# Kernel tuning notes

Hardware: AMD Instinct MI355X
Metric: run time of the kernel (lower is better)

The kernel has to match this reference:

```python
import jax, jax.numpy as jnp
import numpy as np

ALPHA = 0.2  # LeakyReLU negative slope
MASK_VAL = -9e15


def setup_inputs() -> dict:
    key = jax.random.key(0)
    k1, k2, k3, k4 = jax.random.split(key, 4)
    N, F_in, F_out = 8192, 512, 128
    h = jax.random.normal(k1, (N, F_in), dtype=jnp.float32)
    adj = jax.random.randint(k2, (N, N), 0, 2, dtype=jnp.int32)
    w = jax.random.normal(k3, (F_in, F_out), dtype=jnp.float32) * 0.05
    a = jax.random.normal(k4, (2 * F_out, 1), dtype=jnp.float32) * 0.05
    return {"h": h, "adj": adj, "w": w, "a": a}


def reference(h, adj, w, a):
    F_out = w.shape[1]
    Wh = h @ w                                  # [N, F_out]
    Wh1 = Wh @ a[:F_out, :]                     # [N, 1]
    Wh2 = Wh @ a[F_out:, :]                     # [N, 1]
    e = Wh1 + Wh2.T                             # [N, N] broadcast additive score
    e = jnp.where(e > 0, e, ALPHA * e)          # LeakyReLU
    att = jnp.where(adj > 0, e, MASK_VAL)       # mask non-edges
    att = jax.nn.softmax(att, axis=1)           # row softmax
    # dropout is identity in eval mode
    h_prime = att @ Wh                          # [N, F_out]
    return jax.nn.elu(h_prime)                  # concat=True -> ELU
```

## Files before the change

kernel.cpp:

```cpp
#include <hip/hip_runtime.h>
#include <hip/hip_bf16.h>

#define LRELU_ALPHA 0.2f

constexpr int N   = 8192;
constexpr int FIN = 512;
constexpr int F   = 128;
constexpr int BRW = 16;
constexpr int BR  = 64;
constexpr int BK  = 64;

typedef __attribute__((ext_vector_type(4))) float f32x4;
typedef __attribute__((ext_vector_type(8))) short s16x8;
typedef __attribute__((ext_vector_type(4))) short s16x4;
typedef __attribute__((ext_vector_type(4))) int   i32x4;
typedef unsigned long long u64;

static __device__ __forceinline__ short f2bf(float x) {
  unsigned u = __float_as_uint(x);
  return (short)((u + 0x7fffu + ((u >> 16) & 1u)) >> 16);
}

__global__ __launch_bounds__(256) void k_wh(
    const float* __restrict__ h, const float* __restrict__ w,
    const float* __restrict__ a, __hip_bfloat16* __restrict__ WhbT,
    float* __restrict__ Wh1, float* __restrict__ Wh2) {
  __shared__ float hl[32][68];
  __shared__ float wl[64][128];
  const int t    = threadIdx.x;
  const int i0   = blockIdx.x * 32;
  const int col4 = (t & 31) * 4;
  const int rq   = t >> 5;
  float acc[4][4] = {};

  for (int k0 = 0; k0 < FIN; k0 += 64) {
#pragma unroll
    for (int j = 0; j < 2; ++j) {
      int c = t + 256 * j;
      int r = c >> 4, kq = c & 15;
      *(f32x4*)&hl[r][kq * 4] =
          *(const f32x4*)(h + (size_t)(i0 + r) * FIN + k0 + kq * 4);
    }
#pragma unroll
    for (int j = 0; j < 8; ++j) {
      int c = t + 256 * j;
      int kr = c >> 5, f4 = (c & 31) * 4;
      *(f32x4*)&wl[kr][f4] = *(const f32x4*)(w + (size_t)(k0 + kr) * F + f4);
    }
    __syncthreads();
#pragma unroll 4
    for (int k4 = 0; k4 < 64; k4 += 4) {
      f32x4 wv[4];
#pragma unroll
      for (int u = 0; u < 4; ++u) wv[u] = *(const f32x4*)&wl[k4 + u][col4];
#pragma unroll
      for (int ri = 0; ri < 4; ++ri) {
        f32x4 hv = *(const f32x4*)&hl[rq * 4 + ri][k4];
#pragma unroll
        for (int u = 0; u < 4; ++u) {
#pragma unroll
          for (int ci = 0; ci < 4; ++ci) acc[ri][ci] += hv[u] * wv[u][ci];
        }
      }
    }
    __syncthreads();
  }
#pragma unroll
  for (int ci = 0; ci < 4; ++ci) {
    int f = col4 + ci;
    s16x4 o = {f2bf(acc[0][ci]), f2bf(acc[1][ci]),
               f2bf(acc[2][ci]), f2bf(acc[3][ci])};
    *(s16x4*)((short*)WhbT + (size_t)f * N + i0 + rq * 4) = o;
  }
  f32x4 av1 = *(const f32x4*)(a + col4);
  f32x4 av2 = *(const f32x4*)(a + F + col4);
  float s1[4], s2[4];
#pragma unroll
  for (int ri = 0; ri < 4; ++ri) {
    s1[ri] = acc[ri][0] * av1[0] + acc[ri][1] * av1[1] +
             acc[ri][2] * av1[2] + acc[ri][3] * av1[3];
    s2[ri] = acc[ri][0] * av2[0] + acc[ri][1] * av2[1] +
             acc[ri][2] * av2[2] + acc[ri][3] * av2[3];
  }
#pragma unroll
  for (int off = 1; off < 32; off <<= 1) {
#pragma unroll
    for (int ri = 0; ri < 4; ++ri) {
      s1[ri] += __shfl_xor(s1[ri], off);
      s2[ri] += __shfl_xor(s2[ri], off);
    }
  }
  if ((t & 31) == 0) {
#pragma unroll
    for (int ri = 0; ri < 4; ++ri) {
      Wh1[i0 + rq * 4 + ri] = s1[ri];
      Wh2[i0 + rq * 4 + ri] = s2[ri];
    }
  }
}

template <int KS>
__global__ __launch_bounds__(256) __attribute__((amdgpu_waves_per_eu(1, 4)))
void k_attn(
    const int* __restrict__ adj, const float* __restrict__ Wh1v,
    const float* __restrict__ Wh2v, const __hip_bfloat16* __restrict__ WhbT,
    float* __restrict__ accP, float* __restrict__ lP) {
  constexpr int JW  = N / KS;
  constexpr int NTL = JW / BK;
  __shared__ __align__(16) short Bl[2][F * BK];
  __shared__ u64   ml[BR][NTL];
  __shared__ float w2l[JW];

  const int t   = threadIdx.x;
  const int l   = t & 63;
  const int w   = t >> 6;
  const int r16 = l & 15;
  const int g8  = (l >> 4) * 8;
  const int i0  = blockIdx.x * BR;
  const int s   = blockIdx.y;

  const int row  = i0 + w * BRW + r16;
  const float w1 = Wh1v[row];
  const float* __restrict__ w2p  = Wh2v + (size_t)s * JW;
  const short* __restrict__ bsrc = (const short*)WhbT + (size_t)s * JW;

  int ldsoff[4]; size_t goff[4];
#pragma unroll
  for (int q = 0; q < 4; ++q) {
    int c  = t + 256 * q;
    int fr = c >> 3;
    ldsoff[q] = (c * 16) ^ ((fr & 7) << 4);
    goff[q]   = (size_t)fr * N + (c & 7) * 8;
  }
  const int sw = (r16 & 7) << 4;

  f32x4 acc[8] = {};
  float lsum = 0.f;
  s16x8 sv[4];

#pragma unroll
  for (int q = 0; q < 4; ++q) sv[q] = *(const s16x8*)(bsrc + goff[q]);

  if (t * 4 < JW) *(f32x4*)&w2l[t * 4] = *(const f32x4*)(w2p + t * 4);

  {
    const int* __restrict__ ap = adj + (size_t)(i0 + w * BRW) * N +
                                 (size_t)s * JW;
    for (int r = 0; r < BRW; ++r) {
      const int* __restrict__ rp = ap + (size_t)r * N;
#pragma unroll
      for (int it = 0; it < JW / 512; ++it) {
        int v[8];
#pragma unroll
        for (int k = 0; k < 8; ++k) v[k] = rp[it * 512 + l + k * 64];
        u64 m[8];
#pragma unroll
        for (int k = 0; k < 8; ++k) m[k] = __ballot(v[k] > 0);
        if (l == 0) {
#pragma unroll
          for (int k = 0; k < 8; ++k)
            ml[w * BRW + r][(it * 8 + k) ^ r] = m[k];
        }
      }
    }
  }
#pragma unroll
  for (int q = 0; q < 4; ++q)
    *(s16x8*)((char*)&Bl[0][0] + ldsoff[q]) = sv[q];
  __syncthreads();

  auto scores = [&](int tl, s16x8& af0, s16x8& af1) {
    const u64 m = ml[w * BRW + r16][tl ^ r16];
    const f32x4 y0 = *(const f32x4*)&w2l[tl * BK + g8];
    const f32x4 y1 = *(const f32x4*)&w2l[tl * BK + g8 + 4];
    const f32x4 y2 = *(const f32x4*)&w2l[tl * BK + g8 + 32];
    const f32x4 y3 = *(const f32x4*)&w2l[tl * BK + g8 + 36];
    const unsigned b0 = (unsigned)(m >> g8) & 0xffu;
    const unsigned b1 = (unsigned)(m >> (g8 + 32)) & 0xffu;
    float p[16];
#pragma unroll
    for (int u = 0; u < 4; ++u) {
      float x = w1 + y0[u]; x = fmaxf(x, LRELU_ALPHA * x);
      p[u] = (b0 >> u) & 1u ? __expf(x) : 0.f;
    }
#pragma unroll
    for (int u = 0; u < 4; ++u) {
      float x = w1 + y1[u]; x = fmaxf(x, LRELU_ALPHA * x);
      p[4 + u] = (b0 >> (4 + u)) & 1u ? __expf(x) : 0.f;
    }
#pragma unroll
    for (int u = 0; u < 4; ++u) {
      float x = w1 + y2[u]; x = fmaxf(x, LRELU_ALPHA * x);
      p[8 + u] = (b1 >> u) & 1u ? __expf(x) : 0.f;
    }
#pragma unroll
    for (int u = 0; u < 4; ++u) {
      float x = w1 + y3[u]; x = fmaxf(x, LRELU_ALPHA * x);
      p[12 + u] = (b1 >> (4 + u)) & 1u ? __expf(x) : 0.f;
    }
#pragma unroll
    for (int u = 0; u < 16; ++u) lsum += p[u];
    af0 = s16x8{f2bf(p[0]),  f2bf(p[1]),  f2bf(p[2]),  f2bf(p[3]),
                f2bf(p[4]),  f2bf(p[5]),  f2bf(p[6]),  f2bf(p[7])};
    af1 = s16x8{f2bf(p[8]),  f2bf(p[9]),  f2bf(p[10]), f2bf(p[11]),
                f2bf(p[12]), f2bf(p[13]), f2bf(p[14]), f2bf(p[15])};
  };

  auto mfma_tile = [&](const char* pb, s16x8 af0, s16x8 af1) {
#pragma unroll
    for (int nb = 0; nb < 8; ++nb) {
      const int rbase = (nb * 16 + r16) * 128;
      s16x8 b0 = *(const s16x8*)(pb + rbase + ((g8 * 2) ^ sw));
      s16x8 b1 = *(const s16x8*)(pb + rbase + ((g8 * 2 + 64) ^ sw));
      acc[nb] = __builtin_amdgcn_mfma_f32_16x16x32_bf16(af0, b0, acc[nb], 0, 0, 0);
      acc[nb] = __builtin_amdgcn_mfma_f32_16x16x32_bf16(af1, b1, acc[nb], 0, 0, 0);
    }
  };

  for (int tl = 0; tl < NTL; tl += 2) {
    {
      const size_t tn = (size_t)(tl + 1) * BK;
#pragma unroll
      for (int q = 0; q < 4; ++q)
        sv[q] = *(const s16x8*)(bsrc + goff[q] + tn);
      s16x8 af0, af1;
      scores(tl, af0, af1);
#pragma unroll
      for (int q = 0; q < 4; ++q)
        *(s16x8*)((char*)&Bl[1][0] + ldsoff[q]) = sv[q];
      mfma_tile((const char*)&Bl[0][0], af0, af1);
    }
    __syncthreads();
    {
      const size_t tn = (size_t)(tl + 2 < NTL ? tl + 2 : tl) * BK;
#pragma unroll
      for (int q = 0; q < 4; ++q)
        sv[q] = *(const s16x8*)(bsrc + goff[q] + tn);
      s16x8 af0, af1;
      scores(tl + 1, af0, af1);
#pragma unroll
      for (int q = 0; q < 4; ++q)
        *(s16x8*)((char*)&Bl[0][0] + ldsoff[q]) = sv[q];
      mfma_tile((const char*)&Bl[1][0], af0, af1);
    }
    __syncthreads();
  }

  lsum += __shfl_xor(lsum, 16);
  lsum += __shfl_xor(lsum, 32);
  if (l < 16) lP[(size_t)s * N + row] = lsum;
  float* op = accP + (size_t)s * N * F;
#pragma unroll
  for (int nb = 0; nb < 8; ++nb) {
#pragma unroll
    for (int rg = 0; rg < 4; ++rg) {
      int r = i0 + w * BRW + (l >> 4) * 4 + rg;
      op[(size_t)r * F + nb * 16 + r16] = acc[nb][rg];
    }
  }
}

template <int KS>
__global__ __launch_bounds__(256) void k_comb(
    const float* __restrict__ accP, const float* __restrict__ lP,
    float* __restrict__ out) {
  const int idx = blockIdx.x * 256 + threadIdx.x;
  const int i   = idx >> 5;
  f32x4 v = {};
  float lt = 0.f;
#pragma unroll
  for (int s = 0; s < KS; ++s) {
    v += *(const f32x4*)(accP + (size_t)s * N * F + (size_t)idx * 4);
    lt += lP[(size_t)s * N + i];
  }
  f32x4 o;
#pragma unroll
  for (int u = 0; u < 4; ++u) {
    float x = v[u] / lt;
    o[u] = x > 0.f ? x : __expf(x) - 1.f;
  }
  *(f32x4*)(out + (size_t)idx * 4) = o;
}

extern "C" void kernel_launch(void* const* d_in, const int* in_sizes, int n_in,
                              void* d_out, int out_size, void* d_ws, size_t ws_size,
                              hipStream_t stream) {
  const float* h   = (const float*)d_in[0];
  const int*   adj = (const int*)d_in[1];
  const float* w   = (const float*)d_in[2];
  const float* a   = (const float*)d_in[3];
  float* out = (float*)d_out;

  char* ws = (char*)d_ws;
  __hip_bfloat16* WhbT = (__hip_bfloat16*)ws;
  float* Wh1 = (float*)(ws + (size_t)F * N * 2);
  float* Wh2 = Wh1 + N;
  float* lP  = Wh2 + N;

  const size_t fixed = (size_t)F * N * 2 + 2 * (size_t)N * 4;
  const size_t need8 = fixed + 8 * (size_t)N * 4 + 8 * (size_t)N * F * 4;

  k_wh<<<N / 32, 256, 0, stream>>>(h, w, a, WhbT, Wh1, Wh2);
  if (ws_size >= need8) {
    constexpr int KS = 8;
    float* accP = lP + (size_t)KS * N;
    k_attn<KS><<<dim3(N / BR, KS), 256, 0, stream>>>(adj, Wh1, Wh2, WhbT,
                                                     accP, lP);
    k_comb<KS><<<(N * F / 4) / 256, 256, 0, stream>>>(accP, lP, out);
  } else {
    constexpr int KS = 4;
    float* accP = lP + (size_t)KS * N;
    k_attn<KS><<<dim3(N / BR, KS), 256, 0, stream>>>(adj, Wh1, Wh2, WhbT,
                                                     accP, lP);
    k_comb<KS><<<(N * F / 4) / 256, 256, 0, stream>>>(accP, lP, out);
  }
}
```

Baseline: 132.9 us.

## Stream adjacency mask per tile inside attention loop and widen Wh projection blocks

```diff
diff --git a/kernel.cpp b/kernel.cpp
--- a/kernel.cpp
+++ b/kernel.cpp
@@ -13,7 +13,6 @@
 typedef __attribute__((ext_vector_type(4))) float f32x4;
 typedef __attribute__((ext_vector_type(8))) short s16x8;
 typedef __attribute__((ext_vector_type(4))) short s16x4;
-typedef __attribute__((ext_vector_type(4))) int   i32x4;
 typedef unsigned long long u64;
 
 static __device__ __forceinline__ short f2bf(float x) {
@@ -21,7 +20,7 @@
   return (short)((u + 0x7fffu + ((u >> 16) & 1u)) >> 16);
 }
 
-__global__ __launch_bounds__(256) void k_wh(
+__global__ __launch_bounds__(512) void k_wh(
     const float* __restrict__ h, const float* __restrict__ w,
     const float* __restrict__ a, __hip_bfloat16* __restrict__ WhbT,
     float* __restrict__ Wh1, float* __restrict__ Wh2) {
@@ -31,19 +30,14 @@
   const int i0   = blockIdx.x * 32;
   const int col4 = (t & 31) * 4;
   const int rq   = t >> 5;
-  float acc[4][4] = {};
+  float acc[2][4] = {};
 
   for (int k0 = 0; k0 < FIN; k0 += 64) {
-#pragma unroll
-    for (int j = 0; j < 2; ++j) {
-      int c = t + 256 * j;
-      int r = c >> 4, kq = c & 15;
-      *(f32x4*)&hl[r][kq * 4] =
-          *(const f32x4*)(h + (size_t)(i0 + r) * FIN + k0 + kq * 4);
-    }
-#pragma unroll
-    for (int j = 0; j < 8; ++j) {
-      int c = t + 256 * j;
+    *(f32x4*)&hl[t >> 4][(t & 15) * 4] =
+        *(const f32x4*)(h + (size_t)(i0 + (t >> 4)) * FIN + k0 + (t & 15) * 4);
+#pragma unroll
+    for (int j = 0; j < 4; ++j) {
+      int c = t + 512 * j;
       int kr = c >> 5, f4 = (c & 31) * 4;
       *(f32x4*)&wl[kr][f4] = *(const f32x4*)(w + (size_t)(k0 + kr) * F + f4);
     }
@@ -54,8 +48,8 @@
 #pragma unroll
       for (int u = 0; u < 4; ++u) wv[u] = *(const f32x4*)&wl[k4 + u][col4];
 #pragma unroll
-      for (int ri = 0; ri < 4; ++ri) {
-        f32x4 hv = *(const f32x4*)&hl[rq * 4 + ri][k4];
+      for (int ri = 0; ri < 2; ++ri) {
+        f32x4 hv = *(const f32x4*)&hl[rq * 2 + ri][k4];
 #pragma unroll
         for (int u = 0; u < 4; ++u) {
 #pragma unroll
@@ -68,15 +62,15 @@
 #pragma unroll
   for (int ci = 0; ci < 4; ++ci) {
     int f = col4 + ci;
-    s16x4 o = {f2bf(acc[0][ci]), f2bf(acc[1][ci]),
-               f2bf(acc[2][ci]), f2bf(acc[3][ci])};
-    *(s16x4*)((short*)WhbT + (size_t)f * N + i0 + rq * 4) = o;
+    unsigned pk = (unsigned)(unsigned short)f2bf(acc[0][ci]) |
+                  ((unsigned)(unsigned short)f2bf(acc[1][ci]) << 16);
+    *(unsigned*)((short*)WhbT + (size_t)f * N + i0 + rq * 2) = pk;
   }
   f32x4 av1 = *(const f32x4*)(a + col4);
   f32x4 av2 = *(const f32x4*)(a + F + col4);
-  float s1[4], s2[4];
-#pragma unroll
-  for (int ri = 0; ri < 4; ++ri) {
+  float s1[2], s2[2];
+#pragma unroll
+  for (int ri = 0; ri < 2; ++ri) {
     s1[ri] = acc[ri][0] * av1[0] + acc[ri][1] * av1[1] +
              acc[ri][2] * av1[2] + acc[ri][3] * av1[3];
     s2[ri] = acc[ri][0] * av2[0] + acc[ri][1] * av2[1] +
@@ -85,16 +79,16 @@
 #pragma unroll
   for (int off = 1; off < 32; off <<= 1) {
 #pragma unroll
-    for (int ri = 0; ri < 4; ++ri) {
+    for (int ri = 0; ri < 2; ++ri) {
       s1[ri] += __shfl_xor(s1[ri], off);
       s2[ri] += __shfl_xor(s2[ri], off);
     }
   }
   if ((t & 31) == 0) {
 #pragma unroll
-    for (int ri = 0; ri < 4; ++ri) {
-      Wh1[i0 + rq * 4 + ri] = s1[ri];
-      Wh2[i0 + rq * 4 + ri] = s2[ri];
+    for (int ri = 0; ri < 2; ++ri) {
+      Wh1[i0 + rq * 2 + ri] = s1[ri];
+      Wh2[i0 + rq * 2 + ri] = s2[ri];
     }
   }
 }
@@ -108,7 +102,7 @@
   constexpr int JW  = N / KS;
   constexpr int NTL = JW / BK;
   __shared__ __align__(16) short Bl[2][F * BK];
-  __shared__ u64   ml[BR][NTL];
+  __shared__ u64   ml[BR][5];
   __shared__ float w2l[JW];
 
   const int t   = threadIdx.x;
@@ -121,6 +115,8 @@
 
   const int row  = i0 + w * BRW + r16;
   const float w1 = Wh1v[row];
+  const int* __restrict__ rp_w   = adj + (size_t)(i0 + w * BRW) * N +
+                                   (size_t)s * JW;
   const float* __restrict__ w2p  = Wh2v + (size_t)s * JW;
   const short* __restrict__ bsrc = (const short*)WhbT + (size_t)s * JW;
 
@@ -137,40 +133,25 @@
   f32x4 acc[8] = {};
   float lsum = 0.f;
   s16x8 sv[4];
-
-#pragma unroll
-  for (int q = 0; q < 4; ++q) sv[q] = *(const s16x8*)(bsrc + goff[q]);
-
-  if (t * 4 < JW) *(f32x4*)&w2l[t * 4] = *(const f32x4*)(w2p + t * 4);
-
-  {
-    const int* __restrict__ ap = adj + (size_t)(i0 + w * BRW) * N +
-                                 (size_t)s * JW;
-    for (int r = 0; r < BRW; ++r) {
-      const int* __restrict__ rp = ap + (size_t)r * N;
-#pragma unroll
-      for (int it = 0; it < JW / 512; ++it) {
-        int v[8];
-#pragma unroll
-        for (int k = 0; k < 8; ++k) v[k] = rp[it * 512 + l + k * 64];
-        u64 m[8];
-#pragma unroll
-        for (int k = 0; k < 8; ++k) m[k] = __ballot(v[k] > 0);
-        if (l == 0) {
-#pragma unroll
-          for (int k = 0; k < 8; ++k)
-            ml[w * BRW + r][(it * 8 + k) ^ r] = m[k];
-        }
-      }
-    }
-  }
-#pragma unroll
-  for (int q = 0; q < 4; ++q)
-    *(s16x8*)((char*)&Bl[0][0] + ldsoff[q]) = sv[q];
-  __syncthreads();
+  int bufA[16], bufB[16];
+
+  auto adj_issue = [&](int (&vv)[16], int tile) {
+#pragma unroll
+    for (int r = 0; r < 16; ++r)
+      vv[r] = rp_w[(size_t)r * N + (size_t)tile * BK + l];
+  };
+  auto ballot_write = [&](const int (&vv)[16], int c) {
+    u64 msk = 0;
+#pragma unroll
+    for (int r = 0; r < 16; ++r) {
+      u64 m = __ballot(vv[r] > 0);
+      if (l == r) msk = m;
+    }
+    if (l < 16) ml[w * BRW + l][c & 3] = msk;
+  };
 
   auto scores = [&](int tl, s16x8& af0, s16x8& af1) {
-    const u64 m = ml[w * BRW + r16][tl ^ r16];
+    const u64 m = ml[w * BRW + r16][tl & 3];
     const f32x4 y0 = *(const f32x4*)&w2l[tl * BK + g8];
     const f32x4 y1 = *(const f32x4*)&w2l[tl * BK + g8 + 4];
     const f32x4 y2 = *(const f32x4*)&w2l[tl * BK + g8 + 32];
@@ -217,14 +198,27 @@
     }
   };
 
+  for (int j4 = t; j4 * 4 < JW; j4 += 256)
+    *(f32x4*)&w2l[j4 * 4] = *(const f32x4*)(w2p + j4 * 4);
+#pragma unroll
+  for (int q = 0; q < 4; ++q) sv[q] = *(const s16x8*)(bsrc + goff[q]);
+  adj_issue(bufB, 0);
+  adj_issue(bufA, 1);
+  ballot_write(bufB, 0);
+#pragma unroll
+  for (int q = 0; q < 4; ++q)
+    *(s16x8*)((char*)&Bl[0][0] + ldsoff[q]) = sv[q];
+  __syncthreads();
+
   for (int tl = 0; tl < NTL; tl += 2) {
     {
-      const size_t tn = (size_t)(tl + 1) * BK;
 #pragma unroll
       for (int q = 0; q < 4; ++q)
-        sv[q] = *(const s16x8*)(bsrc + goff[q] + tn);
+        sv[q] = *(const s16x8*)(bsrc + goff[q] + (size_t)(tl + 1) * BK);
+      if (tl + 2 < NTL) adj_issue(bufB, tl + 2);
       s16x8 af0, af1;
       scores(tl, af0, af1);
+      ballot_write(bufA, tl + 1);
 #pragma unroll
       for (int q = 0; q < 4; ++q)
         *(s16x8*)((char*)&Bl[1][0] + ldsoff[q]) = sv[q];
@@ -236,8 +230,10 @@
 #pragma unroll
       for (int q = 0; q < 4; ++q)
         sv[q] = *(const s16x8*)(bsrc + goff[q] + tn);
+      if (tl + 3 < NTL) adj_issue(bufA, tl + 3);
       s16x8 af0, af1;
       scores(tl + 1, af0, af1);
+      if (tl + 2 < NTL) ballot_write(bufB, tl + 2);
 #pragma unroll
       for (int q = 0; q < 4; ++q)
         *(s16x8*)((char*)&Bl[0][0] + ldsoff[q]) = sv[q];
@@ -300,7 +296,7 @@
   const size_t fixed = (size_t)F * N * 2 + 2 * (size_t)N * 4;
   const size_t need8 = fixed + 8 * (size_t)N * 4 + 8 * (size_t)N * F * 4;
 
-  k_wh<<<N / 32, 256, 0, stream>>>(h, w, a, WhbT, Wh1, Wh2);
+  k_wh<<<N / 32, 512, 0, stream>>>(h, w, a, WhbT, Wh1, Wh2);
   if (ws_size >= need8) {
     constexpr int KS = 8;
     float* accP = lP + (size_t)KS * N;
```

Result: slower. 140.5 us (+5.7%).
